# Optimization experiments

Hardware: AMD Instinct MI355X
Metric: run time of the kernel (lower is better)

The kernel has to match this reference:

```python
import jax, jax.numpy as jnp
import numpy as np

N, D, S, K = 4096, 256, 32, 4   # nodes, in_dim(=out_dim), subspace_dim, num_heads
ETA = 0.5
LAMBDA_SPARSE = 0.05
EDGE_P = 0.02  # graph density for the random adjacency mask


def setup_inputs() -> dict:
    key = jax.random.key(0)
    k1, k2, k3 = jax.random.split(key, 3)
    H = jax.random.normal(k1, (N, D), dtype=jnp.float32)
    # binary adjacency mask with self-loops, stored as float (matches torch usage)
    mask = (jax.random.uniform(k2, (N, N)) < EDGE_P).astype(jnp.float32)
    adj_mask = jnp.maximum(mask, jnp.eye(N, dtype=jnp.float32))
    # per-head orthonormal subspace bases U[k] = qr(randn(D,S)) -> [K, D, S]
    raw = jax.random.normal(k3, (K, D, S), dtype=jnp.float32)
    U, _ = jnp.linalg.qr(raw)
    log_precision = jnp.zeros((K, S), dtype=jnp.float32)
    threshold = jnp.full((D,), LAMBDA_SPARSE, dtype=jnp.float32)
    return {"H": H, "adj_mask": adj_mask, "U": U,
            "log_precision": log_precision, "threshold": threshold}


def reference(H, adj_mask, U, log_precision, threshold):
    s = U.shape[-1]
    inv_sqrt_s = 1.0 / jnp.sqrt(jnp.asarray(s, dtype=H.dtype))
    neg = (1.0 - adj_mask) * (-1e9)  # [N, N] additive mask

    # scan over heads keeps peak memory at one [N,N] score matrix at a time
    def head_step(agg, xs):
        Uk, lpk = xs                       # [D,S], [S]
        Z = H @ Uk                         # [N,S]  (= Zk^T in the torch code)
        Zs = Z * jnp.exp(lpk)              # precision-scaled
        scores = (Zs @ Z.T) * inv_sqrt_s + neg   # [N,N]
        alpha = jax.nn.softmax(scores, axis=-1)
        agg = agg + (alpha @ Z) @ Uk.T     # [N,D] == (Uk @ (Zk @ alpha^T))^T
        return agg, None

    agg, _ = jax.lax.scan(head_step, jnp.zeros_like(H), (U, log_precision))
    H_half = H + ETA * agg                 # in_dim == out_dim -> no proj

    # soft threshold
    H_out = jnp.sign(H_half) * jax.nn.relu(jnp.abs(H_half) - threshold[None, :])

    # orthogonality loss: sum_k ||Uk^T Uk - I||_F^2 + sum_{k<l} ||Uk^T Ul||_F^2
    C = jnp.einsum('kda,ldb->klab', U, U)  # [K,K,S,S] gram blocks (K,S small)
    Kh = U.shape[0]
    I = jnp.eye(s, dtype=U.dtype)
    diag_blocks = C[jnp.arange(Kh), jnp.arange(Kh)]          # [K,S,S]
    orth_loss = ((diag_blocks - I) ** 2).sum()
    upper = jnp.triu(jnp.ones((Kh, Kh), dtype=U.dtype), 1)[:, :, None, None]
    orth_loss = orth_loss + ((C ** 2) * upper).sum()
    return H_out, orth_loss
```

## Files before the change

kernel.cpp:

```cpp
#include <hip/hip_runtime.h>
#include <math.h>

constexpr int NN = 4096;
constexpr int DD = 256;
constexpr int SS = 32;
constexpr int KK = 4;
constexpr int MAXN = 192;
constexpr int SEGMAX = 96;
constexpr float ETA = 0.5f;

#define MEMFENCE() __asm__ volatile("" ::: "memory")

typedef float nfloat4 __attribute__((ext_vector_type(4)));
__device__ __forceinline__ float4 ntload4(const float4* p) {
  nfloat4 v = __builtin_nontemporal_load((const nfloat4*)p);
  float4 r; r.x = v.x; r.y = v.y; r.z = v.z; r.w = v.w;
  return r;
}

__global__ __launch_bounds__(256) void prep_kernel(
    const float* __restrict__ H, const float* __restrict__ U,
    const float* __restrict__ lp, float* __restrict__ Z,
    float* __restrict__ elp, float* __restrict__ lossp) {
  __shared__ float Hl[16][DD];
  __shared__ float red[4];
  const int tid = threadIdx.x;

  if (blockIdx.x < 1024) {
    const int k = blockIdx.x & 3;
    const int n0 = (blockIdx.x >> 2) * 16;

    const float4* H4 = (const float4*)(H + (size_t)n0 * DD);
    float4* Hl4 = (float4*)&Hl[0][0];
    for (int i = tid; i < 16 * DD / 4; i += 256) Hl4[i] = H4[i];
    __syncthreads();

    const int s = tid & 31;
    const int n_l = (tid >> 5) & 7;
    const float* Uk = U + (size_t)k * DD * SS;
    float acc0 = 0.f, acc1 = 0.f;
#pragma unroll 4
    for (int dq = 0; dq < DD / 4; dq++) {
      const float4 h0 = Hl4[n_l * (DD / 4) + dq];
      const float4 h1 = Hl4[(n_l + 8) * (DD / 4) + dq];
      const float u0 = Uk[(4 * dq + 0) * SS + s];
      const float u1 = Uk[(4 * dq + 1) * SS + s];
      const float u2 = Uk[(4 * dq + 2) * SS + s];
      const float u3 = Uk[(4 * dq + 3) * SS + s];
      acc0 += h0.x * u0 + h0.y * u1 + h0.z * u2 + h0.w * u3;
      acc1 += h1.x * u0 + h1.y * u1 + h1.z * u2 + h1.w * u3;
    }
    Z[((size_t)k * NN + n0 + n_l) * SS + s] = acc0;
    Z[((size_t)k * NN + n0 + n_l + 8) * SS + s] = acc1;
  } else {
    const int pair = blockIdx.x - 1024;
    if (pair == 0 && tid < KK * SS) elp[tid] = expf(lp[tid]);
    const int pk[10] = {0, 0, 0, 0, 1, 1, 1, 2, 2, 3};
    const int pl[10] = {0, 1, 2, 3, 1, 2, 3, 2, 3, 3};
    const int k = pk[pair], l = pl[pair];
    const int b = tid & 31;
    const int a0 = tid >> 5;
    float4 acc = {0.f, 0.f, 0.f, 0.f};
    const float4* Uk4 = (const float4*)(U + (size_t)k * DD * SS);
    const float* Ul = U + (size_t)l * DD * SS;
    for (int d = 0; d < DD; d++) {
      const float ub = Ul[(size_t)d * SS + b];
      const float4 ua = Uk4[d * (SS / 4) + a0];
      acc.x += ua.x * ub; acc.y += ua.y * ub;
      acc.z += ua.z * ub; acc.w += ua.w * ub;
    }
    const int abase = 4 * a0;
    float cvx = acc.x - ((k == l && abase + 0 == b) ? 1.0f : 0.0f);
    float cvy = acc.y - ((k == l && abase + 1 == b) ? 1.0f : 0.0f);
    float cvz = acc.z - ((k == l && abase + 2 == b) ? 1.0f : 0.0f);
    float cvw = acc.w - ((k == l && abase + 3 == b) ? 1.0f : 0.0f);
    float tot = cvx * cvx + cvy * cvy + cvz * cvz + cvw * cvw;
#pragma unroll
    for (int off = 32; off >= 1; off >>= 1) tot += __shfl_xor(tot, off);
    if ((tid & 63) == 0) red[tid >> 6] = tot;
    __syncthreads();
    if (tid == 0) lossp[pair] = red[0] + red[1] + red[2] + red[3];
  }
}

__global__ __launch_bounds__(256) void attn_epi(
    const float* __restrict__ mask, const float* __restrict__ Z,
    const float* __restrict__ elp, const float* __restrict__ lossp,
    const float* __restrict__ H, const float* __restrict__ U,
    const float* __restrict__ thr, float* __restrict__ Hout,
    float* __restrict__ loss) {
  const int tid = threadIdx.x;
  const int wv = tid >> 6;
  const int lane = tid & 63;
  const int bid = blockIdx.x;

  __shared__ int segn[4][SEGMAX];
  __shared__ int segc[4];
  __shared__ int nbr[MAXN];
  __shared__ float AOl[4][KK * SS];

  if (bid == 0 && tid == 0) {
    float t = 0.f;
#pragma unroll
    for (int i = 0; i < 10; i++) t += lossp[i];
    loss[0] = t;
  }

  const int p_sub = lane >> 3;
  const int sq = lane & 7;
  const float inv_sqrt_s = 0.17677669529663687f;
  const unsigned long long lt = (1ULL << lane) - 1ULL;
  const int k = wv;
  const float* Zk = Z + (size_t)k * NN * SS;

  for (int r = 0; r < 4; r++) {
    const int row = bid * 4 + r;
    if (r) __syncthreads();

    const float4* m4 = (const float4*)(mask + (size_t)row * NN);
    int cnt = 0;
#pragma unroll
    for (int it = 0; it < 4; it++) {
      const int i = wv * 256 + it * 64 + lane;
      const float4 v = ntload4(&m4[i]);
      unsigned long long bb;
      bb = __ballot(v.x > 0.5f);
      if (v.x > 0.5f) { const int p = cnt + (int)__popcll(bb & lt); if (p < SEGMAX) segn[wv][p] = 4 * i; }
      cnt += (int)__popcll(bb);
      bb = __ballot(v.y > 0.5f);
      if (v.y > 0.5f) { const int p = cnt + (int)__popcll(bb & lt); if (p < SEGMAX) segn[wv][p] = 4 * i + 1; }
      cnt += (int)__popcll(bb);
      bb = __ballot(v.z > 0.5f);
      if (v.z > 0.5f) { const int p = cnt + (int)__popcll(bb & lt); if (p < SEGMAX) segn[wv][p] = 4 * i + 2; }
      cnt += (int)__popcll(bb);
      bb = __ballot(v.w > 0.5f);
      if (v.w > 0.5f) { const int p = cnt + (int)__popcll(bb & lt); if (p < SEGMAX) segn[wv][p] = 4 * i + 3; }
      cnt += (int)__popcll(bb);
    }
    if (lane == 0) segc[wv] = min(cnt, SEGMAX);
    MEMFENCE();
    __syncthreads();

    const int c0 = segc[0], c1 = segc[1], c2 = segc[2], c3 = segc[3];
    const int offs[4] = {0, c0, c0 + c1, c0 + c1 + c2};
    const int c = min(c0 + c1 + c2 + c3, MAXN);
    const int myc = segc[wv];
    const int myoff = offs[wv];
    for (int i = lane; i < myc; i += 64) {
      const int p = myoff + i;
      if (p < MAXN) nbr[p] = segn[wv][i];
    }
    MEMFENCE();
    __syncthreads();

    float4 q4;
    {
      const float4 a = ((const float4*)(Z + ((size_t)k * NN + row) * SS))[sq];
      const float4 e = ((const float4*)(elp + k * SS))[sq];
      q4.x = a.x * e.x; q4.y = a.y * e.y; q4.z = a.z * e.z; q4.w = a.w * e.w;
    }

    float m = -3.0e38f;
    float wsum = 0.f;
    float4 o4 = {0.f, 0.f, 0.f, 0.f};

    bool aA = p_sub < c, aB = (p_sub + 8) < c;
    float4 zA = {0.f, 0.f, 0.f, 0.f}, zB = {0.f, 0.f, 0.f, 0.f};
    if (aA) zA = ((const float4*)(Zk + (size_t)nbr[p_sub] * SS))[sq];
    if (aB) zB = ((const float4*)(Zk + (size_t)nbr[p_sub + 8] * SS))[sq];

    for (int p0 = 0; p0 < c; p0 += 16) {
      const int pa_n = p0 + 16 + p_sub;
      const int pb_n = pa_n + 8;
      const bool aA_n = pa_n < c, aB_n = pb_n < c;
      float4 zA_n = {0.f, 0.f, 0.f, 0.f}, zB_n = {0.f, 0.f, 0.f, 0.f};
      if (aA_n) zA_n = ((const float4*)(Zk + (size_t)nbr[pa_n] * SS))[sq];
      if (aB_n) zB_n = ((const float4*)(Zk + (size_t)nbr[pb_n] * SS))[sq];

      float dA = q4.x * zA.x + q4.y * zA.y + q4.z * zA.z + q4.w * zA.w;
      float dB = q4.x * zB.x + q4.y * zB.y + q4.z * zB.z + q4.w * zB.w;
      dA += __shfl_xor(dA, 1); dB += __shfl_xor(dB, 1);
      dA += __shfl_xor(dA, 2); dB += __shfl_xor(dB, 2);
      dA += __shfl_xor(dA, 4); dB += __shfl_xor(dB, 4);
      dA = aA ? dA * inv_sqrt_s : -3.0e38f;
      dB = aB ? dB * inv_sqrt_s : -3.0e38f;
      float cm = fmaxf(dA, dB);
      cm = fmaxf(cm, __shfl_xor(cm, 8));
      cm = fmaxf(cm, __shfl_xor(cm, 16));
      cm = fmaxf(cm, __shfl_xor(cm, 32));
      const float mn = fmaxf(m, cm);
      const float sc = __expf(m - mn);
      m = mn;
      const float wA = __expf(dA - m);
      const float wB = __expf(dB - m);
      o4.x = o4.x * sc + wA * zA.x + wB * zB.x;
      o4.y = o4.y * sc + wA * zA.y + wB * zB.y;
      o4.z = o4.z * sc + wA * zA.z + wB * zB.z;
      o4.w = o4.w * sc + wA * zA.w + wB * zB.w;
      wsum = wsum * sc + wA + wB;

      zA = zA_n; zB = zB_n; aA = aA_n; aB = aB_n;
    }
#pragma unroll
    for (int off = 8; off <= 32; off <<= 1) {
      o4.x += __shfl_xor(o4.x, off);
      o4.y += __shfl_xor(o4.y, off);
      o4.z += __shfl_xor(o4.z, off);
      o4.w += __shfl_xor(o4.w, off);
      wsum += __shfl_xor(wsum, off);
    }
    const float invl = 1.0f / wsum;
    if (p_sub == 0) {
      float4 o;
      o.x = o4.x * invl; o.y = o4.y * invl;
      o.z = o4.z * invl; o.w = o4.w * invl;
      ((float4*)&AOl[r][0])[k * 8 + sq] = o;
    }
  }
  MEMFENCE();
  __syncthreads();

  {
    const int r0 = bid * 4;
    const int d = tid;
    float acc[4] = {0.f, 0.f, 0.f, 0.f};
    const float4* U4 = (const float4*)U;
    const float4* AOl4 = (const float4*)&AOl[0][0];
#pragma unroll
    for (int kk = 0; kk < KK; kk++) {
      const int ubase = (kk * DD + d) * (SS / 4);
#pragma unroll
      for (int sq2 = 0; sq2 < SS / 4; sq2++) {
        const float4 u = U4[ubase + sq2];
#pragma unroll
        for (int r = 0; r < 4; r++) {
          const float4 a = AOl4[r * (KK * SS / 4) + kk * (SS / 4) + sq2];
          acc[r] += u.x * a.x + u.y * a.y + u.z * a.z + u.w * a.w;
        }
      }
    }
    const float tv = thr[d];
#pragma unroll
    for (int r = 0; r < 4; r++) {
      const float h =
          __builtin_nontemporal_load(&H[(size_t)(r0 + r) * DD + d]) + ETA * acc[r];
      const float ab = fabsf(h) - tv;
      const float o = (ab > 0.0f) ? copysignf(ab, h) : 0.0f;
      __builtin_nontemporal_store(o, &Hout[(size_t)(r0 + r) * DD + d]);
    }
  }
}

extern "C" void kernel_launch(void* const* d_in, const int* in_sizes, int n_in,
                              void* d_out, int out_size, void* d_ws, size_t ws_size,
                              hipStream_t stream) {
  const float* H    = (const float*)d_in[0];
  const float* mask = (const float*)d_in[1];
  const float* U    = (const float*)d_in[2];
  const float* lp   = (const float*)d_in[3];
  const float* thr  = (const float*)d_in[4];

  float* Hout = (float*)d_out;
  float* loss = Hout + (size_t)NN * DD;

  float* Z     = (float*)d_ws;
  float* elp   = Z + (size_t)KK * NN * SS;
  float* lossp = elp + KK * SS;

  prep_kernel<<<1034, 256, 0, stream>>>(H, U, lp, Z, elp, lossp);
  attn_epi<<<NN / 4, 256, 0, stream>>>(mask, Z, elp, lossp, H, U, thr, Hout, loss);
}
```

Baseline: 164.4 us.

## Batch mask loads for two rows per block and double the grid

The attention kernel now handles two rows per block instead of four, which doubles the grid to 2048 blocks. It issues the mask loads for both rows up front, before any ballot compaction, so the memory latency overlaps instead of being paid row by row. Neighbor lists for both rows are built with one pair of barriers rather than a pair per row. Launch bounds ask for higher occupancy. In exchange, U is reloaded for each output row pair in the epilogue and register pressure rises from holding eight float4 values.

```diff
diff --git a/kernel.cpp b/kernel.cpp
--- a/kernel.cpp
+++ b/kernel.cpp
@@ -8,6 +8,7 @@
 constexpr int MAXN = 192;
 constexpr int SEGMAX = 96;
 constexpr float ETA = 0.5f;
+constexpr int RPB = 2;
 
 #define MEMFENCE() __asm__ volatile("" ::: "memory")
 
@@ -83,7 +84,7 @@
   }
 }
 
-__global__ __launch_bounds__(256) void attn_epi(
+__global__ __launch_bounds__(256, 8) void attn_epi(
     const float* __restrict__ mask, const float* __restrict__ Z,
     const float* __restrict__ elp, const float* __restrict__ lossp,
     const float* __restrict__ H, const float* __restrict__ U,
@@ -94,10 +95,10 @@
   const int lane = tid & 63;
   const int bid = blockIdx.x;
 
-  __shared__ int segn[4][SEGMAX];
-  __shared__ int segc[4];
-  __shared__ int nbr[MAXN];
-  __shared__ float AOl[4][KK * SS];
+  __shared__ int segn[RPB][4][SEGMAX];
+  __shared__ int segc[RPB][4];
+  __shared__ int nbr[RPB][MAXN];
+  __shared__ float AOl[RPB][KK * SS];
 
   if (bid == 0 && tid == 0) {
     float t = 0.f;
@@ -105,53 +106,74 @@
     for (int i = 0; i < 10; i++) t += lossp[i];
     loss[0] = t;
   }
+
+  const unsigned long long lt = (1ULL << lane) - 1ULL;
+
+  {
+    const float4* m4 = (const float4*)(mask + (size_t)(bid * RPB) * NN);
+    const int base = wv * 256 + lane;
+    float4 v[RPB][4];
+#pragma unroll
+    for (int r = 0; r < RPB; r++)
+#pragma unroll
+      for (int it = 0; it < 4; it++)
+        v[r][it] = ntload4(&m4[(size_t)r * (NN / 4) + base + it * 64]);
+
+#pragma unroll
+    for (int r = 0; r < RPB; r++) {
+      int cnt = 0;
+#pragma unroll
+      for (int it = 0; it < 4; it++) {
+        const int i = base + it * 64;
+        const float4 vv = v[r][it];
+        unsigned long long bb;
+        bb = __ballot(vv.x > 0.5f);
+        if (vv.x > 0.5f) { const int p = cnt + (int)__popcll(bb & lt); if (p < SEGMAX) segn[r][wv][p] = 4 * i; }
+        cnt += (int)__popcll(bb);
+        bb = __ballot(vv.y > 0.5f);
+        if (vv.y > 0.5f) { const int p = cnt + (int)__popcll(bb & lt); if (p < SEGMAX) segn[r][wv][p] = 4 * i + 1; }
+        cnt += (int)__popcll(bb);
+        bb = __ballot(vv.z > 0.5f);
+        if (vv.z > 0.5f) { const int p = cnt + (int)__popcll(bb & lt); if (p < SEGMAX) segn[r][wv][p] = 4 * i + 2; }
+        cnt += (int)__popcll(bb);
+        bb = __ballot(vv.w > 0.5f);
+        if (vv.w > 0.5f) { const int p = cnt + (int)__popcll(bb & lt); if (p < SEGMAX) segn[r][wv][p] = 4 * i + 3; }
+        cnt += (int)__popcll(bb);
+      }
+      if (lane == 0) segc[r][wv] = min(cnt, SEGMAX);
+    }
+  }
+  MEMFENCE();
+  __syncthreads();
+
+  int ctot[RPB];
+#pragma unroll
+  for (int r = 0; r < RPB; r++) {
+    const int c0 = segc[r][0], c1 = segc[r][1];
+    const int c2 = segc[r][2], c3 = segc[r][3];
+    const int offs[4] = {0, c0, c0 + c1, c0 + c1 + c2};
+    ctot[r] = min(c0 + c1 + c2 + c3, MAXN);
+    const int myc = segc[r][wv];
+    const int myoff = offs[wv];
+    for (int i = lane; i < myc; i += 64) {
+      const int p = myoff + i;
+      if (p < MAXN) nbr[r][p] = segn[r][wv][i];
+    }
+  }
+  MEMFENCE();
+  __syncthreads();
 
   const int p_sub = lane >> 3;
   const int sq = lane & 7;
   const float inv_sqrt_s = 0.17677669529663687f;
-  const unsigned long long lt = (1ULL << lane) - 1ULL;
   const int k = wv;
   const float* Zk = Z + (size_t)k * NN * SS;
 
-  for (int r = 0; r < 4; r++) {
-    const int row = bid * 4 + r;
-    if (r) __syncthreads();
-
-    const float4* m4 = (const float4*)(mask + (size_t)row * NN);
-    int cnt = 0;
-#pragma unroll
-    for (int it = 0; it < 4; it++) {
-      const int i = wv * 256 + it * 64 + lane;
-      const float4 v = ntload4(&m4[i]);
-      unsigned long long bb;
-      bb = __ballot(v.x > 0.5f);
-      if (v.x > 0.5f) { const int p = cnt + (int)__popcll(bb & lt); if (p < SEGMAX) segn[wv][p] = 4 * i; }
-      cnt += (int)__popcll(bb);
-      bb = __ballot(v.y > 0.5f);
-      if (v.y > 0.5f) { const int p = cnt + (int)__popcll(bb & lt); if (p < SEGMAX) segn[wv][p] = 4 * i + 1; }
-      cnt += (int)__popcll(bb);
-      bb = __ballot(v.z > 0.5f);
-      if (v.z > 0.5f) { const int p = cnt + (int)__popcll(bb & lt); if (p < SEGMAX) segn[wv][p] = 4 * i + 2; }
-      cnt += (int)__popcll(bb);
-      bb = __ballot(v.w > 0.5f);
-      if (v.w > 0.5f) { const int p = cnt + (int)__popcll(bb & lt); if (p < SEGMAX) segn[wv][p] = 4 * i + 3; }
-      cnt += (int)__popcll(bb);
-    }
-    if (lane == 0) segc[wv] = min(cnt, SEGMAX);
-    MEMFENCE();
-    __syncthreads();
-
-    const int c0 = segc[0], c1 = segc[1], c2 = segc[2], c3 = segc[3];
-    const int offs[4] = {0, c0, c0 + c1, c0 + c1 + c2};
-    const int c = min(c0 + c1 + c2 + c3, MAXN);
-    const int myc = segc[wv];
-    const int myoff = offs[wv];
-    for (int i = lane; i < myc; i += 64) {
-      const int p = myoff + i;
-      if (p < MAXN) nbr[p] = segn[wv][i];
-    }
-    MEMFENCE();
-    __syncthreads();
+#pragma unroll
+  for (int r = 0; r < RPB; r++) {
+    const int row = bid * RPB + r;
+    const int c = ctot[r];
+    const int* nb = &nbr[r][0];
 
     float4 q4;
     {
@@ -166,16 +188,16 @@
 
     bool aA = p_sub < c, aB = (p_sub + 8) < c;
     float4 zA = {0.f, 0.f, 0.f, 0.f}, zB = {0.f, 0.f, 0.f, 0.f};
-    if (aA) zA = ((const float4*)(Zk + (size_t)nbr[p_sub] * SS))[sq];
-    if (aB) zB = ((const float4*)(Zk + (size_t)nbr[p_sub + 8] * SS))[sq];
+    if (aA) zA = ((const float4*)(Zk + (size_t)nb[p_sub] * SS))[sq];
+    if (aB) zB = ((const float4*)(Zk + (size_t)nb[p_sub + 8] * SS))[sq];
 
     for (int p0 = 0; p0 < c; p0 += 16) {
       const int pa_n = p0 + 16 + p_sub;
       const int pb_n = pa_n + 8;
       const bool aA_n = pa_n < c, aB_n = pb_n < c;
       float4 zA_n = {0.f, 0.f, 0.f, 0.f}, zB_n = {0.f, 0.f, 0.f, 0.f};
-      if (aA_n) zA_n = ((const float4*)(Zk + (size_t)nbr[pa_n] * SS))[sq];
-      if (aB_n) zB_n = ((const float4*)(Zk + (size_t)nbr[pb_n] * SS))[sq];
+      if (aA_n) zA_n = ((const float4*)(Zk + (size_t)nb[pa_n] * SS))[sq];
+      if (aB_n) zB_n = ((const float4*)(Zk + (size_t)nb[pb_n] * SS))[sq];
 
       float dA = q4.x * zA.x + q4.y * zA.y + q4.z * zA.z + q4.w * zA.w;
       float dB = q4.x * zB.x + q4.y * zB.y + q4.z * zB.z + q4.w * zB.w;
@@ -221,9 +243,11 @@
   __syncthreads();
 
   {
-    const int r0 = bid * 4;
+    const int r0 = bid * RPB;
     const int d = tid;
-    float acc[4] = {0.f, 0.f, 0.f, 0.f};
+    float acc[RPB];
+#pragma unroll
+    for (int r = 0; r < RPB; r++) acc[r] = 0.f;
     const float4* U4 = (const float4*)U;
     const float4* AOl4 = (const float4*)&AOl[0][0];
 #pragma unroll
@@ -233,7 +257,7 @@
       for (int sq2 = 0; sq2 < SS / 4; sq2++) {
         const float4 u = U4[ubase + sq2];
 #pragma unroll
-        for (int r = 0; r < 4; r++) {
+        for (int r = 0; r < RPB; r++) {
           const float4 a = AOl4[r * (KK * SS / 4) + kk * (SS / 4) + sq2];
           acc[r] += u.x * a.x + u.y * a.y + u.z * a.z + u.w * a.w;
         }
@@ -241,7 +265,7 @@
     }
     const float tv = thr[d];
 #pragma unroll
-    for (int r = 0; r < 4; r++) {
+    for (int r = 0; r < RPB; r++) {
       const float h =
           __builtin_nontemporal_load(&H[(size_t)(r0 + r) * DD + d]) + ETA * acc[r];
       const float ab = fabsf(h) - tv;
@@ -268,5 +292,5 @@
   float* lossp = elp + KK * SS;
 
   prep_kernel<<<1034, 256, 0, stream>>>(H, U, lp, Z, elp, lossp);
-  attn_epi<<<NN / 4, 256, 0, stream>>>(mask, Z, elp, lossp, H, U, thr, Hout, loss);
-}
+  attn_epi<<<NN / RPB, 256, 0, stream>>>(mask, Z, elp, lossp, H, U, thr, Hout, loss);
+}
```

Result: slower. 175.9 us (+7.0%).
